# Optimization experiments

Hardware: AMD Instinct MI355X
Metric: run time of the kernel (lower is better)

## Reference

```python
import jax, jax.numpy as jnp
import numpy as np


def setup_inputs() -> dict:
    key = jax.random.key(0)
    B, F = 16384, 4096
    x = jax.random.normal(key, (B, F), dtype=jnp.float32)
    return {"x": x, "k": 64}


def reference(x, k):
    # top-k along dim=1 (last axis for 2D input)
    _, idx = jax.lax.top_k(x, k)                      # idx: [B, k]
    B = x.shape[0]
    rows = jnp.arange(B)[:, None]                     # [B, 1]
    mask = jnp.zeros_like(x).at[rows, idx].set(1.0)   # scatter ones at top-k positions
    return x * mask
```

## Files before the change

kernel.cpp:

```cpp
#include <hip/hip_runtime.h>
#include <stdint.h>

#define TK_F       4096
#define TK_THREADS 256
#define TK_EPT     16
#define TK_NBINS   2048
#define TK_CAP     1024

__device__ __forceinline__ unsigned int tk_f2u(unsigned int b) {
    return b ^ ((unsigned int)(((int)b) >> 31) | 0x80000000u);
}
__device__ __forceinline__ unsigned int tk_u2f(unsigned int u) {
    return u ^ ((~(unsigned int)(((int)u) >> 31)) | 0x80000000u);
}

__global__ __launch_bounds__(TK_THREADS, 4)
void tk_topk_mask(const float* __restrict__ x, const int* __restrict__ kp,
                  float* __restrict__ out, int B)
{
    __shared__ unsigned int hist[TK_NBINS];
    __shared__ unsigned int cand[TK_CAP];
    __shared__ unsigned int waveTot[TK_THREADS / 64];
    __shared__ unsigned int sh_cnt;
    __shared__ int          sh_b;
    __shared__ unsigned int sh_cum;
    __shared__ unsigned int sh_T, sh_g, sh_e;

    const int tid = threadIdx.x;
    const int row = blockIdx.x;
    if (row >= B) return;
    const unsigned int k = (unsigned int)kp[0];

    const unsigned int* xr  = (const unsigned int*)(x + (size_t)row * TK_F);
    unsigned int*       orow = (unsigned int*)(out + (size_t)row * TK_F);

    for (int i = tid; i < TK_NBINS; i += TK_THREADS) hist[i] = 0u;
    if (tid == 0) { sh_cnt = 0u; sh_b = -1; }

    unsigned int u[TK_EPT];
    const uint4* xv = (const uint4*)xr;
    #pragma unroll
    for (int v = 0; v < 4; ++v) {
        uint4 q = xv[tid + v * TK_THREADS];
        u[v*4+0] = tk_f2u(q.x);
        u[v*4+1] = tk_f2u(q.y);
        u[v*4+2] = tk_f2u(q.z);
        u[v*4+3] = tk_f2u(q.w);
    }
    __syncthreads();

    #pragma unroll
    for (int e = 0; e < TK_EPT; ++e)
        atomicAdd(&hist[u[e] >> 21], 1u);
    __syncthreads();

    unsigned int hbin[8];
    unsigned int s = 0;
    const int base = tid * 8;
    #pragma unroll
    for (int j = 0; j < 8; ++j) { hbin[j] = hist[base + j]; s += hbin[j]; }

    unsigned int acc = s;
    const int lane = tid & 63;
    #pragma unroll
    for (int d = 1; d < 64; d <<= 1) {
        unsigned int v = (unsigned int)__shfl_down((int)acc, d, 64);
        if (lane + d < 64) acc += v;
    }
    const int wid = tid >> 6;
    if (lane == 0) waveTot[wid] = acc;
    __syncthreads();
    unsigned int later = 0;
    #pragma unroll
    for (int w = 0; w < TK_THREADS / 64; ++w)
        if (w > wid) later += waveTot[w];

    unsigned int run = later + (acc - s);
    #pragma unroll
    for (int j = 7; j >= 0; --j) {
        unsigned int h = hbin[j];
        if (run < k && run + h >= k) { sh_b = base + j; sh_cum = run; }
        run += h;
    }
    __syncthreads();

    const int b = sh_b;
    if (b < 0) {
        #pragma unroll
        for (int v = 0; v < 4; ++v) {
            uint4 q;
            q.x = tk_u2f(u[v*4+0]); q.y = tk_u2f(u[v*4+1]);
            q.z = tk_u2f(u[v*4+2]); q.w = tk_u2f(u[v*4+3]);
            ((uint4*)orow)[tid + v * TK_THREADS] = q;
        }
        return;
    }
    const unsigned int cum = sh_cum;

    #pragma unroll
    for (int e = 0; e < TK_EPT; ++e) {
        if ((int)(u[e] >> 21) == b) {
            unsigned int p = atomicAdd(&sh_cnt, 1u);
            if (p < TK_CAP) cand[p] = u[e];
        }
    }
    __syncthreads();

    const unsigned int L = (sh_cnt < TK_CAP) ? sh_cnt : TK_CAP;
    const unsigned int r = k - cum;
    for (unsigned int j = tid; j < L; j += TK_THREADS) {
        unsigned int uj = cand[j];
        unsigned int g = 0, eq = 0;
        for (unsigned int i = 0; i < L; ++i) {
            unsigned int ui = cand[i];
            g  += (ui > uj)  ? 1u : 0u;
            eq += (ui == uj) ? 1u : 0u;
        }
        if (g < r && g + eq >= r) { sh_T = uj; sh_g = g; sh_e = eq; }
    }
    __syncthreads();

    const unsigned int T  = sh_T;
    const unsigned int re = r - sh_g;
    const unsigned int ce = sh_e;
    const bool easy = (ce == re);

    #pragma unroll
    for (int v = 0; v < 4; ++v) {
        uint4 q;
        #pragma unroll
        for (int j = 0; j < 4; ++j) {
            unsigned int uu  = u[v*4+j];
            unsigned int val = 0u;
            if (uu > T) {
                val = tk_u2f(uu);
            } else if (uu == T) {
                if (easy) {
                    val = tk_u2f(uu);
                } else {
                    int idx = (tid + v * TK_THREADS) * 4 + j;
                    unsigned int cnt = 0;
                    for (int i = 0; i < idx; ++i)
                        cnt += (tk_f2u(xr[i]) == T) ? 1u : 0u;
                    if (cnt < re) val = tk_u2f(uu);
                }
            }
            (&q.x)[j] = val;
        }
        ((uint4*)orow)[tid + v * TK_THREADS] = q;
    }
}

extern "C" void kernel_launch(void* const* d_in, const int* in_sizes, int n_in,
                              void* d_out, int out_size, void* d_ws, size_t ws_size,
                              hipStream_t stream) {
    const float* x  = (const float*)d_in[0];
    const int*   kp = (const int*)d_in[1];
    float*       out = (float*)d_out;
    const int B = in_sizes[0] / TK_F;
    hipLaunchKernelGGL(tk_topk_mask, dim3(B), dim3(TK_THREADS), 0, stream,
                       x, kp, out, B);
}
```

Measured before the change: 541.8 us.

## Process one row per wavefront with multi-pass radix select instead of candidate sort

Each 64-lane wavefront now owns a whole row, keeping 64 values per lane in registers. Block-wide barriers are replaced by wave-local LDS fences and shuffles. The O(L^2) candidate comparison is replaced by a 11+7+7+7 bit radix select that finds the exact threshold. This removes block synchronisation and the quadratic candidate scan. In exchange, register pressure rises sharply (64 values per lane) and each wave does more serial atomic histogram passes, which may reduce occupancy.

```diff
diff --git a/kernel.cpp b/kernel.cpp
--- a/kernel.cpp
+++ b/kernel.cpp
@@ -2,162 +2,182 @@
 #include <stdint.h>
 
 #define TK_F       4096
-#define TK_THREADS 256
-#define TK_EPT     16
-#define TK_NBINS   2048
-#define TK_CAP     1024
+#define TK_RPB     4
+#define TK_THREADS (TK_RPB * 64)
 
-__device__ __forceinline__ unsigned int tk_f2u(unsigned int b) {
-    return b ^ ((unsigned int)(((int)b) >> 31) | 0x80000000u);
+__device__ __forceinline__ unsigned tk_f2u(unsigned b) {
+    return b ^ ((unsigned)(((int)b) >> 31) | 0x80000000u);
 }
-__device__ __forceinline__ unsigned int tk_u2f(unsigned int u) {
-    return u ^ ((~(unsigned int)(((int)u) >> 31)) | 0x80000000u);
+__device__ __forceinline__ unsigned tk_u2f(unsigned u) {
+    return u ^ ((~(unsigned)(((int)u) >> 31)) | 0x80000000u);
+}
+
+__device__ __forceinline__ void tk_lds_fence() {
+    __asm__ volatile("s_waitcnt lgkmcnt(0)" ::: "memory");
+}
+
+__device__ __attribute__((noinline))
+unsigned tk_count_eq_before(const unsigned* __restrict__ xr, int idx, unsigned T) {
+    unsigned c = 0;
+    for (int i = 0; i < idx; ++i) c += (tk_f2u(xr[i]) == T) ? 1u : 0u;
+    return c;
 }
 
 __global__ __launch_bounds__(TK_THREADS, 4)
 void tk_topk_mask(const float* __restrict__ x, const int* __restrict__ kp,
                   float* __restrict__ out, int B)
 {
-    __shared__ unsigned int hist[TK_NBINS];
-    __shared__ unsigned int cand[TK_CAP];
-    __shared__ unsigned int waveTot[TK_THREADS / 64];
-    __shared__ unsigned int sh_cnt;
-    __shared__ int          sh_b;
-    __shared__ unsigned int sh_cum;
-    __shared__ unsigned int sh_T, sh_g, sh_e;
+    __shared__ unsigned hist[TK_RPB][2048];
 
-    const int tid = threadIdx.x;
-    const int row = blockIdx.x;
+    const int lane = threadIdx.x & 63;
+    const int wid  = threadIdx.x >> 6;
+    const int row  = blockIdx.x * TK_RPB + wid;
     if (row >= B) return;
-    const unsigned int k = (unsigned int)kp[0];
 
-    const unsigned int* xr  = (const unsigned int*)(x + (size_t)row * TK_F);
-    unsigned int*       orow = (unsigned int*)(out + (size_t)row * TK_F);
+    const unsigned k = (unsigned)kp[0];
 
-    for (int i = tid; i < TK_NBINS; i += TK_THREADS) hist[i] = 0u;
-    if (tid == 0) { sh_cnt = 0u; sh_b = -1; }
+    const uint4* xv = (const uint4*)(x + (size_t)row * TK_F);
+    uint4*       ov = (uint4*)(out + (size_t)row * TK_F);
 
-    unsigned int u[TK_EPT];
-    const uint4* xv = (const uint4*)xr;
+    unsigned u[64];
     #pragma unroll
-    for (int v = 0; v < 4; ++v) {
-        uint4 q = xv[tid + v * TK_THREADS];
-        u[v*4+0] = tk_f2u(q.x);
-        u[v*4+1] = tk_f2u(q.y);
-        u[v*4+2] = tk_f2u(q.z);
-        u[v*4+3] = tk_f2u(q.w);
+    for (int v = 0; v < 16; ++v) {
+        uint4 q = xv[lane + 64 * v];
+        u[4*v+0] = tk_f2u(q.x); u[4*v+1] = tk_f2u(q.y);
+        u[4*v+2] = tk_f2u(q.z); u[4*v+3] = tk_f2u(q.w);
     }
-    __syncthreads();
 
-    #pragma unroll
-    for (int e = 0; e < TK_EPT; ++e)
-        atomicAdd(&hist[u[e] >> 21], 1u);
-    __syncthreads();
-
-    unsigned int hbin[8];
-    unsigned int s = 0;
-    const int base = tid * 8;
-    #pragma unroll
-    for (int j = 0; j < 8; ++j) { hbin[j] = hist[base + j]; s += hbin[j]; }
-
-    unsigned int acc = s;
-    const int lane = tid & 63;
-    #pragma unroll
-    for (int d = 1; d < 64; d <<= 1) {
-        unsigned int v = (unsigned int)__shfl_down((int)acc, d, 64);
-        if (lane + d < 64) acc += v;
+    if (k == 0) {
+        uint4 z = make_uint4(0u, 0u, 0u, 0u);
+        #pragma unroll
+        for (int v = 0; v < 16; ++v) ov[lane + 64 * v] = z;
+        return;
     }
-    const int wid = tid >> 6;
-    if (lane == 0) waveTot[wid] = acc;
-    __syncthreads();
-    unsigned int later = 0;
-    #pragma unroll
-    for (int w = 0; w < TK_THREADS / 64; ++w)
-        if (w > wid) later += waveTot[w];
-
-    unsigned int run = later + (acc - s);
-    #pragma unroll
-    for (int j = 7; j >= 0; --j) {
-        unsigned int h = hbin[j];
-        if (run < k && run + h >= k) { sh_b = base + j; sh_cum = run; }
-        run += h;
-    }
-    __syncthreads();
-
-    const int b = sh_b;
-    if (b < 0) {
+    if (k >= TK_F) {
         #pragma unroll
-        for (int v = 0; v < 4; ++v) {
+        for (int v = 0; v < 16; ++v) {
             uint4 q;
-            q.x = tk_u2f(u[v*4+0]); q.y = tk_u2f(u[v*4+1]);
-            q.z = tk_u2f(u[v*4+2]); q.w = tk_u2f(u[v*4+3]);
-            ((uint4*)orow)[tid + v * TK_THREADS] = q;
+            q.x = tk_u2f(u[4*v+0]); q.y = tk_u2f(u[4*v+1]);
+            q.z = tk_u2f(u[4*v+2]); q.w = tk_u2f(u[4*v+3]);
+            ov[lane + 64 * v] = q;
         }
         return;
     }
-    const unsigned int cum = sh_cum;
+
+    unsigned* h = &hist[wid][0];
+    unsigned r = k;
+    unsigned prefix = 0;
+    unsigned eTot = 0;
+
+    {
+        uint4 z4 = make_uint4(0u, 0u, 0u, 0u);
+        #pragma unroll
+        for (int i = 0; i < 8; ++i) ((uint4*)h)[lane + 64 * i] = z4;
+        tk_lds_fence();
+
+        #pragma unroll
+        for (int e = 0; e < 64; ++e) atomicAdd(&h[u[e] >> 21], 1u);
+        tk_lds_fence();
+
+        unsigned s = 0;
+        {
+            const uint4* hb = (const uint4*)&h[lane * 32];
+            #pragma unroll
+            for (int i = 0; i < 8; ++i) { uint4 q = hb[i]; s += q.x + q.y + q.z + q.w; }
+        }
+        unsigned acc = s;
+        #pragma unroll
+        for (int d = 1; d < 64; d <<= 1) {
+            unsigned v = (unsigned)__shfl_down((int)acc, d, 64);
+            if (lane + d < 64) acc += v;
+        }
+        unsigned run = acc - s;
+        int fbin = -1; unsigned frun = 0;
+        #pragma unroll
+        for (int j = 31; j >= 0; --j) {
+            unsigned hh = h[lane * 32 + j];
+            if (fbin < 0 && run < r && run + hh >= r) { fbin = lane * 32 + j; frun = run; }
+            run += hh;
+        }
+        unsigned long long m = __ballot(fbin >= 0);
+        int src = __ffsll((unsigned long long)m) - 1;
+        prefix = (unsigned)__shfl(fbin, src, 64);
+        r     -= (unsigned)__shfl((int)frun, src, 64);
+    }
 
     #pragma unroll
-    for (int e = 0; e < TK_EPT; ++e) {
-        if ((int)(u[e] >> 21) == b) {
-            unsigned int p = atomicAdd(&sh_cnt, 1u);
-            if (p < TK_CAP) cand[p] = u[e];
+    for (int l = 0; l < 3; ++l) {
+        const int sm = 21 - 7 * l;
+        const int sd = sm - 7;
+
+        h[lane] = 0u; h[lane + 64] = 0u;
+        tk_lds_fence();
+
+        #pragma unroll
+        for (int e = 0; e < 64; ++e) {
+            if ((u[e] >> sm) == prefix)
+                atomicAdd(&h[(u[e] >> sd) & 127u], 1u);
         }
+        tk_lds_fence();
+
+        unsigned h0 = h[lane * 2], h1 = h[lane * 2 + 1];
+        unsigned ss = h0 + h1;
+        unsigned ac = ss;
+        #pragma unroll
+        for (int d = 1; d < 64; d <<= 1) {
+            unsigned v = (unsigned)__shfl_down((int)ac, d, 64);
+            if (lane + d < 64) ac += v;
+        }
+        unsigned rn = ac - ss;
+        int fd = -1; unsigned fr = 0, fe = 0;
+        if (rn < r && rn + h1 >= r) { fd = lane * 2 + 1; fr = rn; fe = h1; }
+        rn += h1;
+        if (fd < 0 && rn < r && rn + h0 >= r) { fd = lane * 2; fr = rn; fe = h0; }
+
+        unsigned long long m = __ballot(fd >= 0);
+        int src = __ffsll((unsigned long long)m) - 1;
+        unsigned dg = (unsigned)__shfl(fd, src, 64);
+        r    -= (unsigned)__shfl((int)fr, src, 64);
+        eTot  = (unsigned)__shfl((int)fe, src, 64);
+        prefix = (prefix << 7) | dg;
     }
-    __syncthreads();
 
-    const unsigned int L = (sh_cnt < TK_CAP) ? sh_cnt : TK_CAP;
-    const unsigned int r = k - cum;
-    for (unsigned int j = tid; j < L; j += TK_THREADS) {
-        unsigned int uj = cand[j];
-        unsigned int g = 0, eq = 0;
-        for (unsigned int i = 0; i < L; ++i) {
-            unsigned int ui = cand[i];
-            g  += (ui > uj)  ? 1u : 0u;
-            eq += (ui == uj) ? 1u : 0u;
-        }
-        if (g < r && g + eq >= r) { sh_T = uj; sh_g = g; sh_e = eq; }
-    }
-    __syncthreads();
-
-    const unsigned int T  = sh_T;
-    const unsigned int re = r - sh_g;
-    const unsigned int ce = sh_e;
-    const bool easy = (ce == re);
+    const unsigned T  = prefix;
+    const unsigned re = r;
+    const bool easy = (eTot == re);
+    const unsigned* xr = (const unsigned*)(x + (size_t)row * TK_F);
 
     #pragma unroll
-    for (int v = 0; v < 4; ++v) {
+    for (int v = 0; v < 16; ++v) {
         uint4 q;
         #pragma unroll
-        for (int j = 0; j < 4; ++j) {
-            unsigned int uu  = u[v*4+j];
-            unsigned int val = 0u;
+        for (int c = 0; c < 4; ++c) {
+            unsigned uu  = u[4*v + c];
+            unsigned val = 0u;
             if (uu > T) {
                 val = tk_u2f(uu);
             } else if (uu == T) {
                 if (easy) {
                     val = tk_u2f(uu);
                 } else {
-                    int idx = (tid + v * TK_THREADS) * 4 + j;
-                    unsigned int cnt = 0;
-                    for (int i = 0; i < idx; ++i)
-                        cnt += (tk_f2u(xr[i]) == T) ? 1u : 0u;
-                    if (cnt < re) val = tk_u2f(uu);
+                    int idx = 4 * (lane + 64 * v) + c;
+                    if (tk_count_eq_before(xr, idx, T) < re) val = tk_u2f(uu);
                 }
             }
-            (&q.x)[j] = val;
+            (&q.x)[c] = val;
         }
-        ((uint4*)orow)[tid + v * TK_THREADS] = q;
+        ov[lane + 64 * v] = q;
     }
 }
 
 extern "C" void kernel_launch(void* const* d_in, const int* in_sizes, int n_in,
                               void* d_out, int out_size, void* d_ws, size_t ws_size,
                               hipStream_t stream) {
-    const float* x  = (const float*)d_in[0];
-    const int*   kp = (const int*)d_in[1];
-    float*       out = (float*)d_out;
+    const float* x   = (const float*)d_in[0];
+    const int*   kpp = (const int*)d_in[1];
+    float*       o   = (float*)d_out;
     const int B = in_sizes[0] / TK_F;
-    hipLaunchKernelGGL(tk_topk_mask, dim3(B), dim3(TK_THREADS), 0, stream,
-                       x, kp, out, B);
+    const int grid = (B + TK_RPB - 1) / TK_RPB;
+    hipLaunchKernelGGL(tk_topk_mask, dim3(grid), dim3(TK_THREADS), 0, stream,
+                       x, kpp, o, B);
 }
```

New measurement: 714.4 us. +31.8%, slower.
